# Kernel tuning notes

Measured on AMD Instinct MI355X. Metric: run time of the kernel, lower is better.

## Reference

```python
import jax, jax.numpy as jnp
import numpy as np

N, E = 50000, 400000
C_IN, C_OUT = 64, 32
K = 9  # kernel_size 3x3


def _quad_basis(t):
    # open B-spline basis, degree 2, per torch_spline_conv: k_mod in {0,1,2}
    # t = frac(pseudo * (kernel_size - degree)) = pseudo here (kernel_size=3, degree=2)
    return jnp.stack([0.5 * (1.0 - t) ** 2, -t * t + t + 0.5, 0.5 * t * t], axis=-1)  # [E,3]


def spline_basis(pseudo):
    # kernel_size=[3,3], degree=2, open spline: v = p*(3-2)=p, floor(v)=0 for p in [0,1),
    # so weight index for combination s is exactly s = k_mod0 + 3*k_mod1.
    q0 = _quad_basis(pseudo[:, 0])  # [E,3] varies with s%3
    q1 = _quad_basis(pseudo[:, 1])  # [E,3] varies with s//3
    return (q1[:, :, None] * q0[:, None, :]).reshape(-1, K)  # [E,9]


def spline_conv(x, src, dst, B, W, root, bias, n_nodes):
    xj = x[src]  # gather source node features [E,Cin]
    msg = jnp.zeros((xj.shape[0], W.shape[-1]), x.dtype)
    for k in range(K):  # fixed small kernel loop; avoids [E,K,Cin] blowup
        msg = msg + (xj * B[:, k, None]) @ W[k]
    agg = jax.ops.segment_sum(msg, dst, num_segments=n_nodes)  # aggr='add'
    return agg + x @ root + bias


def setup_inputs() -> dict:
    key = jax.random.key(0)
    ks = jax.random.split(key, 10)
    x = jax.random.normal(ks[0], (N, C_IN), jnp.float32)
    edge_index = jax.random.randint(ks[1], (2, E), 0, N, jnp.int64)
    pseudo = jax.random.uniform(ks[2], (E, 2), jnp.float32)
    skip = jax.random.normal(ks[3], (N, C_OUT), jnp.float32)
    s1 = 1.0 / np.sqrt(C_IN)
    s2 = 1.0 / np.sqrt(C_OUT)
    W1 = jax.random.normal(ks[4], (K, C_IN, C_OUT), jnp.float32) * s1
    root1 = jax.random.normal(ks[5], (C_IN, C_OUT), jnp.float32) * s1
    b1 = jnp.zeros((C_OUT,), jnp.float32)
    W2 = jax.random.normal(ks[6], (K, C_OUT, C_OUT), jnp.float32) * s2
    root2 = jax.random.normal(ks[7], (C_OUT, C_OUT), jnp.float32) * s2
    b2 = jnp.zeros((C_OUT,), jnp.float32)
    return {"x": x, "edge_index": edge_index, "pseudo": pseudo, "skip": skip,
            "W1": W1, "root1": root1, "b1": b1, "W2": W2, "root2": root2, "b2": b2}


def reference(x, edge_index, pseudo, skip, W1, root1, b1, W2, root2, b2):
    src, dst = edge_index[0], edge_index[1]  # flow: source_to_target
    B = spline_basis(pseudo)  # [E,9]
    n = x.shape[0]
    h = jax.nn.relu(spline_conv(x, src, dst, B, W1, root1, b1, n))
    h = jnp.concatenate([h, skip], axis=1)  # [N, Cout+Cskip] == [N, Cin]
    h = jax.nn.relu(spline_conv(h, src, dst, B, W1, root1, b1, n))
    h = jax.nn.relu(spline_conv(h, src, dst, B, W2, root2, b2, n))
    return h
```

## Files before the change

kernel.cpp:

```cpp
#include <hip/hip_runtime.h>
#include <hip/hip_bf16.h>


typedef __attribute__((ext_vector_type(8))) short short8;
typedef __attribute__((ext_vector_type(4))) float f32x4;

__device__ __forceinline__ float blo(unsigned u) {
    union { unsigned u; float f; } x; x.u = u << 16; return x.f;
}
__device__ __forceinline__ float bhi(unsigned u) {
    union { unsigned u; float f; } x; x.u = u & 0xffff0000u; return x.f;
}
__device__ __forceinline__ unsigned short f2bf(float f) {
    union { float f; unsigned u; } x; x.f = f;
    unsigned r = x.u + 0x7fffu + ((x.u >> 16) & 1u);
    return (unsigned short)(r >> 16);
}
__device__ __forceinline__ short8 cvt8(const float* p) {
    float4 a = *(const float4*)p;
    float4 b = *(const float4*)(p + 4);
    short8 r;
    r[0] = (short)f2bf(a.x); r[1] = (short)f2bf(a.y);
    r[2] = (short)f2bf(a.z); r[3] = (short)f2bf(a.w);
    r[4] = (short)f2bf(b.x); r[5] = (short)f2bf(b.y);
    r[6] = (short)f2bf(b.z); r[7] = (short)f2bf(b.w);
    return r;
}

#define YROW 296

__device__ __forceinline__ void m_edge(const unsigned short* sY, const float4 r,
                                       uint4* __restrict__ msgOut, int n0, int l)
{
    const int srcl = __float_as_int(r.x) - n0;
    const int dp   = __float_as_int(r.y);
    const float p0 = r.z, p1 = r.w;

    const float qb[3] = {0.5f * (1.f - p0) * (1.f - p0), -p0 * p0 + p0 + 0.5f, 0.5f * p0 * p0};
    const float qa[3] = {0.5f * (1.f - p1) * (1.f - p1), -p1 * p1 + p1 + 0.5f, 0.5f * p1 * p1};

    const uint4* yb = (const uint4*)(sY + srcl * YROW) + l;
    float s[8] = {0.f, 0.f, 0.f, 0.f, 0.f, 0.f, 0.f, 0.f};
    #pragma unroll
    for (int a = 0; a < 3; ++a) {
        float z[8] = {0.f, 0.f, 0.f, 0.f, 0.f, 0.f, 0.f, 0.f};
        #pragma unroll
        for (int b = 0; b < 3; ++b) {
            uint4 v = yb[(a * 3 + b) * 4];
            const float cw = qb[b];
            z[0] = fmaf(cw, blo(v.x), z[0]); z[1] = fmaf(cw, bhi(v.x), z[1]);
            z[2] = fmaf(cw, blo(v.y), z[2]); z[3] = fmaf(cw, bhi(v.y), z[3]);
            z[4] = fmaf(cw, blo(v.z), z[4]); z[5] = fmaf(cw, bhi(v.z), z[5]);
            z[6] = fmaf(cw, blo(v.w), z[6]); z[7] = fmaf(cw, bhi(v.w), z[7]);
        }
        #pragma unroll
        for (int j = 0; j < 8; ++j) s[j] = fmaf(qa[a], z[j], s[j]);
    }

    union { uint4 u; __hip_bfloat162 h[4]; } o;
    #pragma unroll
    for (int j = 0; j < 4; ++j)
        o.h[j] = __float22bfloat162_rn(float2{s[2 * j], s[2 * j + 1]});
    msgOut[(size_t)dp * 4 + l] = o.u;
}

__device__ __forceinline__ void m_phase(const unsigned short* sY,
                                        const int* __restrict__ sstart,
                                        const float4* __restrict__ erec,
                                        uint4* __restrict__ msgOut,
                                        int n0, int t, int N, int E)
{
    const int e0 = sstart[n0];
    const int e1 = (n0 + 32 < N) ? sstart[n0 + 32] : E;
    const int l  = t & 3;

    int e = e0 + (t >> 2);
    if (e >= e1) return;
    float4 r0 = erec[e];
    bool  has1 = (e + 64 < e1);
    float4 r1;
    if (has1) r1 = erec[e + 64];

    while (true) {
        const int ep0 = e + 128, ep1 = e + 192;
        const bool hp0 = ep0 < e1, hp1 = ep1 < e1;
        float4 rp0, rp1;
        if (hp0) rp0 = erec[ep0];
        if (hp1) rp1 = erec[ep1];

        m_edge(sY, r0, msgOut, n0, l);
        if (!has1) break;
        m_edge(sY, r1, msgOut, n0, l);

        if (!hp0) break;
        r0 = rp0; r1 = rp1; has1 = hp1; e = ep0;
    }
}

template<int NHALF>
__device__ __forceinline__ void t_core(short8 a0, short8 a1,
                                       const unsigned short* __restrict__ Wt,
                                       const float* __restrict__ bias,
                                       unsigned short* sY, float* __restrict__ aggOut,
                                       int n0, int rh, int cgp, int lc, int q, int N)
{
    const int CIN = NHALF * 32;
    #pragma unroll
    for (int j = 0; j < 10; ++j) {
        const int ti = cgp * 10 + j;
        const unsigned short* wp = Wt + ((size_t)(ti * 16 + lc)) * CIN + q * 8;
        f32x4 acc = (f32x4){0.f, 0.f, 0.f, 0.f};
        acc = __builtin_amdgcn_mfma_f32_16x16x32_bf16(a0, *(const short8*)wp, acc, 0, 0, 0);
        if (NHALF == 2)
            acc = __builtin_amdgcn_mfma_f32_16x16x32_bf16(a1, *(const short8*)(wp + 32), acc, 0, 0, 0);

        if (ti < 18) {
            #pragma unroll
            for (int r = 0; r < 4; ++r) {
                int nl = rh * 16 + q * 4 + r;
                sY[nl * YROW + ti * 16 + lc] = f2bf(acc[r]);
            }
        } else {
            int c = (ti - 18) * 16 + lc;
            float bv = bias[c];
            #pragma unroll
            for (int r = 0; r < 4; ++r) {
                int n = n0 + rh * 16 + q * 4 + r;
                if (n < N) aggOut[(size_t)n * 32 + c] = acc[r] + bv;
            }
        }
    }
}

__global__ __launch_bounds__(256, 6)
void layer_tm0(const float* __restrict__ Xa,
               const unsigned short* __restrict__ Wt, const float* __restrict__ bias,
               const int* __restrict__ sstart, const float4* __restrict__ erec,
               float* __restrict__ aggOut, uint4* __restrict__ msgOut, int N, int E)
{
    __shared__ __align__(16) unsigned short sY[32 * YROW];
    const int t = threadIdx.x, wv = t >> 6, lane = t & 63;
    const int lc = lane & 15, q = lane >> 4;
    const int rh = wv & 1, cgp = wv >> 1;
    const int n0 = blockIdx.x * 32;

    int na = n0 + rh * 16 + lc;
    if (na >= N) na = N - 1;
    const float* p = Xa + (size_t)na * 64 + q * 8;
    short8 a0 = cvt8(p);
    short8 a1 = cvt8(p + 32);

    t_core<2>(a0, a1, Wt, bias, sY, aggOut, n0, rh, cgp, lc, q, N);
    __syncthreads();
    m_phase(sY, sstart, erec, msgOut, n0, t, N, E);
}

template<int MODE>
__global__ __launch_bounds__(256, 6)
void layer_gtm(const float* __restrict__ aggPrev, const float* __restrict__ skipv,
               const unsigned short* __restrict__ Wt, const float* __restrict__ bias,
               const int* __restrict__ sstart, const int* __restrict__ dstart,
               const float4* __restrict__ erec,
               const uint4* __restrict__ msgIn, uint4* __restrict__ msgOut,
               float* __restrict__ aggOut, int N, int E)
{
    __shared__ __align__(16) unsigned short sY[32 * YROW];
    float* sH = (float*)sY;
    const int t = threadIdx.x, wv = t >> 6, lane = t & 63;
    const int lc = lane & 15, q = lane >> 4;
    const int rh = wv & 1, cgp = wv >> 1;
    const int n0 = blockIdx.x * 32;

    {
        const int nl = t >> 3;
        const int l  = t & 3;
        const int h  = (t >> 2) & 1;
        int n = n0 + nl;
        if (n >= N) n = N - 1;
        float4 A, B;
        if (h == 0) {
            const float* ap = aggPrev + (size_t)n * 32 + l * 8;
            A = *(const float4*)ap;
            B = *(const float4*)(ap + 4);
        } else {
            A = {0.f, 0.f, 0.f, 0.f};
            B = {0.f, 0.f, 0.f, 0.f};
        }
        float4 C = {0.f, 0.f, 0.f, 0.f}, D = {0.f, 0.f, 0.f, 0.f};
        const int e0 = dstart[n] - E;
        const int e1 = ((n + 1 < N) ? dstart[n + 1] : 2 * E) - E;
        const uint4* mp = msgIn + l;
        int e = e0 + h;
        for (; e + 6 < e1; e += 8) {
            uint4 v0 = mp[(size_t)e * 4];
            uint4 v1 = mp[(size_t)(e + 2) * 4];
            uint4 v2 = mp[(size_t)(e + 4) * 4];
            uint4 v3 = mp[(size_t)(e + 6) * 4];
            A.x += blo(v0.x); A.y += bhi(v0.x); A.z += blo(v0.y); A.w += bhi(v0.y);
            B.x += blo(v0.z); B.y += bhi(v0.z); B.z += blo(v0.w); B.w += bhi(v0.w);
            C.x += blo(v1.x); C.y += bhi(v1.x); C.z += blo(v1.y); C.w += bhi(v1.y);
            D.x += blo(v1.z); D.y += bhi(v1.z); D.z += blo(v1.w); D.w += bhi(v1.w);
            A.x += blo(v2.x); A.y += bhi(v2.x); A.z += blo(v2.y); A.w += bhi(v2.y);
            B.x += blo(v2.z); B.y += bhi(v2.z); B.z += blo(v2.w); B.w += bhi(v2.w);
            C.x += blo(v3.x); C.y += bhi(v3.x); C.z += blo(v3.y); C.w += bhi(v3.y);
            D.x += blo(v3.z); D.y += bhi(v3.z); D.z += blo(v3.w); D.w += bhi(v3.w);
        }
        for (; e < e1; e += 2) {
            uint4 v = mp[(size_t)e * 4];
            A.x += blo(v.x); A.y += bhi(v.x); A.z += blo(v.y); A.w += bhi(v.y);
            B.x += blo(v.z); B.y += bhi(v.z); B.z += blo(v.w); B.w += bhi(v.w);
        }
        A.x += C.x; A.y += C.y; A.z += C.z; A.w += C.w;
        B.x += D.x; B.y += D.y; B.z += D.z; B.w += D.w;
        A.x += __shfl_xor(A.x, 4); A.y += __shfl_xor(A.y, 4);
        A.z += __shfl_xor(A.z, 4); A.w += __shfl_xor(A.w, 4);
        B.x += __shfl_xor(B.x, 4); B.y += __shfl_xor(B.y, 4);
        B.z += __shfl_xor(B.z, 4); B.w += __shfl_xor(B.w, 4);
        if (h == 0) {
            float* hp = sH + nl * 33 + l * 8;
            hp[0] = fmaxf(A.x, 0.f); hp[1] = fmaxf(A.y, 0.f);
            hp[2] = fmaxf(A.z, 0.f); hp[3] = fmaxf(A.w, 0.f);
            hp[4] = fmaxf(B.x, 0.f); hp[5] = fmaxf(B.y, 0.f);
            hp[6] = fmaxf(B.z, 0.f); hp[7] = fmaxf(B.w, 0.f);
        }
    }
    __syncthreads();

    const float* hp = sH + (rh * 16 + lc) * 33 + q * 8;
    union { short8 v; __hip_bfloat162 h2[4]; } pk;
    #pragma unroll
    for (int j = 0; j < 4; ++j)
        pk.h2[j] = __float22bfloat162_rn(float2{hp[2 * j], hp[2 * j + 1]});
    short8 a0 = pk.v;
    short8 a1;
    if (MODE == 1) {
        int na = n0 + rh * 16 + lc;
        if (na >= N) na = N - 1;
        a1 = cvt8(skipv + (size_t)na * 32 + q * 8);
    }
    __syncthreads();

    t_core<(MODE == 1) ? 2 : 1>(a0, a1, Wt, bias, sY, aggOut, n0, rh, cgp, lc, q, N);
    __syncthreads();
    m_phase(sY, sstart, erec, msgOut, n0, t, N, E);
}

__global__ __launch_bounds__(256)
void gather_kernel(const int* __restrict__ dstart, const uint4* __restrict__ msg4,
                   float* __restrict__ agg, int N, int E)
{
    const int t = threadIdx.x;
    const int n = blockIdx.x * 32 + (t >> 3);
    if (n >= N) return;
    const int l = t & 3;
    const int h = (t >> 2) & 1;

    const int e0 = dstart[n] - E;
    const int e1 = ((n + 1 < N) ? dstart[n + 1] : 2 * E) - E;

    float4* ap = (float4*)(agg + (size_t)n * 32 + l * 8);
    float4 A, B;
    if (h == 0) { A = ap[0]; B = ap[1]; }
    else { A = {0.f, 0.f, 0.f, 0.f}; B = {0.f, 0.f, 0.f, 0.f}; }
    float4 C = {0.f, 0.f, 0.f, 0.f}, D = {0.f, 0.f, 0.f, 0.f};
    const uint4* mp = msg4 + l;
    int e = e0 + h;
    for (; e + 6 < e1; e += 8) {
        uint4 v0 = mp[(size_t)e * 4];
        uint4 v1 = mp[(size_t)(e + 2) * 4];
        uint4 v2 = mp[(size_t)(e + 4) * 4];
        uint4 v3 = mp[(size_t)(e + 6) * 4];
        A.x += blo(v0.x); A.y += bhi(v0.x); A.z += blo(v0.y); A.w += bhi(v0.y);
        B.x += blo(v0.z); B.y += bhi(v0.z); B.z += blo(v0.w); B.w += bhi(v0.w);
        C.x += blo(v1.x); C.y += bhi(v1.x); C.z += blo(v1.y); C.w += bhi(v1.y);
        D.x += blo(v1.z); D.y += bhi(v1.z); D.z += blo(v1.w); D.w += bhi(v1.w);
        A.x += blo(v2.x); A.y += bhi(v2.x); A.z += blo(v2.y); A.w += bhi(v2.y);
        B.x += blo(v2.z); B.y += bhi(v2.z); B.z += blo(v2.w); B.w += bhi(v2.w);
        C.x += blo(v3.x); C.y += bhi(v3.x); C.z += blo(v3.y); C.w += bhi(v3.y);
        D.x += blo(v3.z); D.y += bhi(v3.z); D.z += blo(v3.w); D.w += bhi(v3.w);
    }
    for (; e < e1; e += 2) {
        uint4 v = mp[(size_t)e * 4];
        A.x += blo(v.x); A.y += bhi(v.x); A.z += blo(v.y); A.w += bhi(v.y);
        B.x += blo(v.z); B.y += bhi(v.z); B.z += blo(v.w); B.w += bhi(v.w);
    }
    A.x += C.x; A.y += C.y; A.z += C.z; A.w += C.w;
    B.x += D.x; B.y += D.y; B.z += D.z; B.w += D.w;
    A.x += __shfl_xor(A.x, 4); A.y += __shfl_xor(A.y, 4);
    A.z += __shfl_xor(A.z, 4); A.w += __shfl_xor(A.w, 4);
    B.x += __shfl_xor(B.x, 4); B.y += __shfl_xor(B.y, 4);
    B.z += __shfl_xor(B.z, 4); B.w += __shfl_xor(B.w, 4);
    if (h == 0) {
        A.x = fmaxf(A.x, 0.f); A.y = fmaxf(A.y, 0.f); A.z = fmaxf(A.z, 0.f); A.w = fmaxf(A.w, 0.f);
        B.x = fmaxf(B.x, 0.f); B.y = fmaxf(B.y, 0.f); B.z = fmaxf(B.z, 0.f); B.w = fmaxf(B.w, 0.f);
        ap[0] = A; ap[1] = B;
    }
}


__global__ __launch_bounds__(256)
void init_kernel(int* __restrict__ hist, int n2,
                 const float* __restrict__ W1, const float* __restrict__ root1,
                 const float* __restrict__ W2, const float* __restrict__ root2,
                 unsigned short* __restrict__ Wt1, unsigned short* __restrict__ Wt2)
{
    int i = blockIdx.x * 256 + threadIdx.x;
    if (i < n2) { hist[i] = 0; return; }
    int j = i - n2;
    if (j < 320 * 64) {
        int col = j / 64, k = j % 64;
        float v = (col < 288) ? W1[((size_t)(col >> 5) * 64 + k) * 32 + (col & 31)]
                              : root1[(size_t)k * 32 + (col - 288)];
        Wt1[j] = f2bf(v);
    } else if (j < 320 * 96) {
        int jj = j - 320 * 64;
        int col = jj / 32, k = jj % 32;
        float v = (col < 288) ? W2[((size_t)(col >> 5) * 32 + k) * 32 + (col & 31)]
                              : root2[(size_t)k * 32 + (col - 288)];
        Wt2[jj] = f2bf(v);
    }
}

__global__ __launch_bounds__(256)
void count_rank_kernel(const int* __restrict__ ei, int* __restrict__ hist,
                       uint2* __restrict__ rank, int N, int E)
{
    int e = blockIdx.x * 256 + threadIdx.x;
    if (e >= E) return;
    unsigned rs = atomicAdd((unsigned*)&hist[ei[e]], 1u);
    unsigned rd = atomicAdd((unsigned*)&hist[N + ei[E + e]], 1u);
    rank[e] = uint2{rs, rd};
}

__global__ __launch_bounds__(1024)
void scan1_kernel(int* __restrict__ hist, int* __restrict__ bsum, int n)
{
    __shared__ int s[1024];
    int tid = threadIdx.x;
    int i = blockIdx.x * 1024 + tid;
    int v = (i < n) ? hist[i] : 0;
    s[tid] = v;
    __syncthreads();
    for (int off = 1; off < 1024; off <<= 1) {
        int add = (tid >= off) ? s[tid - off] : 0;
        __syncthreads();
        s[tid] += add;
        __syncthreads();
    }
    if (i < n) hist[i] = s[tid] - v;
    if (tid == 1023) bsum[blockIdx.x] = s[1023];
}

__global__ __launch_bounds__(1024)
void scan3_kernel(int* __restrict__ hist, const int* __restrict__ bsum, int n)
{
    __shared__ int sred[128];
    int tid = threadIdx.x;
    int b = blockIdx.x;
    if (tid < 128) sred[tid] = (tid < b) ? bsum[tid] : 0;
    __syncthreads();
    for (int off = 64; off > 0; off >>= 1) {
        if (tid < off) sred[tid] += sred[tid + off];
        __syncthreads();
    }
    int pre = sred[0];
    int i = b * 1024 + tid;
    if (i < n) hist[i] += pre;
}

__global__ __launch_bounds__(256)
void scatter_plain_kernel(const int* __restrict__ ei, const float* __restrict__ pseudo,
                          const int* __restrict__ start, const uint2* __restrict__ rank,
                          float4* __restrict__ erec, int N, int E)
{
    int e = blockIdx.x * 256 + threadIdx.x;
    if (e >= E) return;
    int sv = ei[e];
    int dv = ei[E + e];
    uint2 rk = rank[e];
    int ps = start[sv] + (int)rk.x;
    int pd = start[N + dv] + (int)rk.y - E;
    float4 r;
    r.x = __int_as_float(sv);
    r.y = __int_as_float(pd);
    r.z = pseudo[2 * (size_t)e];
    r.w = pseudo[2 * (size_t)e + 1];
    erec[ps] = r;
}

extern "C" void kernel_launch(void* const* d_in, const int* in_sizes, int n_in,
                              void* d_out, int out_size, void* d_ws, size_t ws_size,
                              hipStream_t stream) {
    const float* x      = (const float*)d_in[0];
    const int*   ei     = (const int*)  d_in[1];
    const float* pseudo = (const float*)d_in[2];
    const float* skip   = (const float*)d_in[3];
    const float* W1     = (const float*)d_in[4];
    const float* root1  = (const float*)d_in[5];
    const float* b1     = (const float*)d_in[6];
    const float* W2     = (const float*)d_in[7];
    const float* root2  = (const float*)d_in[8];
    const float* b2     = (const float*)d_in[9];

    const int N = in_sizes[0] / 64;
    const int E = in_sizes[1] / 2;
    float* out = (float*)d_out;

    unsigned short* msgA = (unsigned short*)d_ws;
    unsigned short* msgB = msgA + (size_t)E * 32;
    float*  agg1  = (float*)(msgB + (size_t)E * 32);
    float*  agg2  = agg1 + (size_t)N * 32;
    float4* erec  = (float4*)(agg2 + (size_t)N * 32);
    int*    start = (int*)(erec + E);
    int*    bsum  = start + 2 * N;
    unsigned short* Wt1 = (unsigned short*)(bsum + 256);
    unsigned short* Wt2 = Wt1 + 320 * 64;
    uint2*  rank  = (uint2*)msgB;

    const dim3 blk(256);
    const int tb   = (N + 31) / 32;
    const int gb   = (N + 31) / 32;
    const int e256 = (E + 255) / 256;
    const int n2k  = (2 * N + 1023) / 1024;
    const int itot = 2 * N + 320 * 96;
    int* dstart = start + N;

    init_kernel<<<(itot + 255) / 256, blk, 0, stream>>>(start, 2 * N, W1, root1, W2, root2, Wt1, Wt2);
    count_rank_kernel<<<e256, blk, 0, stream>>>(ei, start, rank, N, E);
    scan1_kernel<<<n2k, 1024, 0, stream>>>(start, bsum, 2 * N);
    scan3_kernel<<<n2k, 1024, 0, stream>>>(start, bsum, 2 * N);
    scatter_plain_kernel<<<e256, blk, 0, stream>>>(ei, pseudo, start, rank, erec, N, E);

    layer_tm0<<<tb, blk, 0, stream>>>(x, Wt1, b1, start, erec, agg1, (uint4*)msgA, N, E);
    layer_gtm<1><<<tb, blk, 0, stream>>>(agg1, skip, Wt1, b1, start, dstart, erec,
                                         (const uint4*)msgA, (uint4*)msgB, agg2, N, E);
    layer_gtm<2><<<tb, blk, 0, stream>>>(agg2, nullptr, Wt2, b2, start, dstart, erec,
                                         (const uint4*)msgB, (uint4*)msgA, out, N, E);
    gather_kernel<<<gb, blk, 0, stream>>>(dstart, (const uint4*)msgA, out, N, E);
}
```

Baseline: 226.0 us.

## Split fused transform+message kernels into separate transform and message kernels via global Y buffer

Each layer's fused kernel, which computed the per-node transformed features into shared memory and then emitted per-edge messages, is split in two. One kernel writes the bf16 transformed features to a global buffer, and a separate kernel reloads them into shared memory before running the message phase. This lowers per-kernel shared memory and register pressure, and the launch bounds are raised to allow more resident blocks. The cost is extra global traffic for the roughly N×288 bf16 buffer plus three additional kernel launches.

After: 264.8 us. 1.17x slower.

```diff
diff --git a/kernel.cpp b/kernel.cpp
--- a/kernel.cpp
+++ b/kernel.cpp
@@ -28,6 +28,7 @@
 }
 
 #define YROW 296
+#define YGR  288
 
 __device__ __forceinline__ void m_edge(const unsigned short* sY, const float4 r,
                                        uint4* __restrict__ msgOut, int n0, int l)
@@ -98,11 +99,12 @@
 }
 
 template<int NHALF>
-__device__ __forceinline__ void t_core(short8 a0, short8 a1,
-                                       const unsigned short* __restrict__ Wt,
-                                       const float* __restrict__ bias,
-                                       unsigned short* sY, float* __restrict__ aggOut,
-                                       int n0, int rh, int cgp, int lc, int q, int N)
+__device__ __forceinline__ void t_core_g(short8 a0, short8 a1,
+                                         const unsigned short* __restrict__ Wt,
+                                         const float* __restrict__ bias,
+                                         unsigned short* __restrict__ ybuf,
+                                         float* __restrict__ aggOut,
+                                         int n0, int rh, int cgp, int lc, int q, int N)
 {
     const int CIN = NHALF * 32;
     #pragma unroll
@@ -117,8 +119,8 @@
         if (ti < 18) {
             #pragma unroll
             for (int r = 0; r < 4; ++r) {
-                int nl = rh * 16 + q * 4 + r;
-                sY[nl * YROW + ti * 16 + lc] = f2bf(acc[r]);
+                int n = n0 + rh * 16 + q * 4 + r;
+                if (n < N) ybuf[(size_t)n * YGR + ti * 16 + lc] = f2bf(acc[r]);
             }
         } else {
             int c = (ti - 18) * 16 + lc;
@@ -132,13 +134,11 @@
     }
 }
 
-__global__ __launch_bounds__(256, 6)
-void layer_tm0(const float* __restrict__ Xa,
-               const unsigned short* __restrict__ Wt, const float* __restrict__ bias,
-               const int* __restrict__ sstart, const float4* __restrict__ erec,
-               float* __restrict__ aggOut, uint4* __restrict__ msgOut, int N, int E)
-{
-    __shared__ __align__(16) unsigned short sY[32 * YROW];
+__global__ __launch_bounds__(256, 8)
+void layer_t0(const float* __restrict__ Xa,
+              const unsigned short* __restrict__ Wt, const float* __restrict__ bias,
+              unsigned short* __restrict__ ybuf, float* __restrict__ aggOut, int N)
+{
     const int t = threadIdx.x, wv = t >> 6, lane = t & 63;
     const int lc = lane & 15, q = lane >> 4;
     const int rh = wv & 1, cgp = wv >> 1;
@@ -150,22 +150,19 @@
     short8 a0 = cvt8(p);
     short8 a1 = cvt8(p + 32);
 
-    t_core<2>(a0, a1, Wt, bias, sY, aggOut, n0, rh, cgp, lc, q, N);
-    __syncthreads();
-    m_phase(sY, sstart, erec, msgOut, n0, t, N, E);
+    t_core_g<2>(a0, a1, Wt, bias, ybuf, aggOut, n0, rh, cgp, lc, q, N);
 }
 
 template<int MODE>
-__global__ __launch_bounds__(256, 6)
-void layer_gtm(const float* __restrict__ aggPrev, const float* __restrict__ skipv,
-               const unsigned short* __restrict__ Wt, const float* __restrict__ bias,
-               const int* __restrict__ sstart, const int* __restrict__ dstart,
-               const float4* __restrict__ erec,
-               const uint4* __restrict__ msgIn, uint4* __restrict__ msgOut,
-               float* __restrict__ aggOut, int N, int E)
-{
-    __shared__ __align__(16) unsigned short sY[32 * YROW];
-    float* sH = (float*)sY;
+__global__ __launch_bounds__(256, 8)
+void layer_gt(const float* __restrict__ aggPrev, const float* __restrict__ skipv,
+              const unsigned short* __restrict__ Wt, const float* __restrict__ bias,
+              const int* __restrict__ dstart,
+              const uint4* __restrict__ msgIn,
+              unsigned short* __restrict__ ybuf, float* __restrict__ aggOut,
+              int N, int E)
+{
+    __shared__ __align__(16) float sH[32 * 33];
     const int t = threadIdx.x, wv = t >> 6, lane = t & 63;
     const int lc = lane & 15, q = lane >> 4;
     const int rh = wv & 1, cgp = wv >> 1;
@@ -238,10 +235,31 @@
         if (na >= N) na = N - 1;
         a1 = cvt8(skipv + (size_t)na * 32 + q * 8);
     }
+
+    t_core_g<(MODE == 1) ? 2 : 1>(a0, a1, Wt, bias, ybuf, aggOut, n0, rh, cgp, lc, q, N);
+}
+
+__global__ __launch_bounds__(256, 8)
+void layer_m(const unsigned short* __restrict__ ybuf,
+             const int* __restrict__ sstart, const float4* __restrict__ erec,
+             uint4* __restrict__ msgOut, int N, int E)
+{
+    __shared__ __align__(16) unsigned short sY[32 * YROW];
+    const int t = threadIdx.x;
+    const int n0 = blockIdx.x * 32;
+
+    #pragma unroll
+    for (int k = 0; k < 9; ++k) {
+        int idx = t + k * 256;
+        int row = idx / 72;
+        int c2  = idx - row * 72;
+        int n = n0 + row;
+        if (n >= N) n = N - 1;
+        *(uint2*)(sY + row * YROW + c2 * 4) =
+            *(const uint2*)(ybuf + (size_t)n * YGR + c2 * 4);
+    }
     __syncthreads();
 
-    t_core<(MODE == 1) ? 2 : 1>(a0, a1, Wt, bias, sY, aggOut, n0, rh, cgp, lc, q, N);
-    __syncthreads();
     m_phase(sY, sstart, erec, msgOut, n0, t, N, E);
 }
 
@@ -408,7 +426,8 @@
 
     unsigned short* msgA = (unsigned short*)d_ws;
     unsigned short* msgB = msgA + (size_t)E * 32;
-    float*  agg1  = (float*)(msgB + (size_t)E * 32);
+    unsigned short* ybuf = msgB + (size_t)E * 32;
+    float*  agg1  = (float*)(ybuf + (size_t)N * YGR);
     float*  agg2  = agg1 + (size_t)N * 32;
     float4* erec  = (float4*)(agg2 + (size_t)N * 32);
     int*    start = (int*)(erec + E);
@@ -431,10 +450,13 @@
     scan3_kernel<<<n2k, 1024, 0, stream>>>(start, bsum, 2 * N);
     scatter_plain_kernel<<<e256, blk, 0, stream>>>(ei, pseudo, start, rank, erec, N, E);
 
-    layer_tm0<<<tb, blk, 0, stream>>>(x, Wt1, b1, start, erec, agg1, (uint4*)msgA, N, E);
-    layer_gtm<1><<<tb, blk, 0, stream>>>(agg1, skip, Wt1, b1, start, dstart, erec,
-                                         (const uint4*)msgA, (uint4*)msgB, agg2, N, E);
-    layer_gtm<2><<<tb, blk, 0, stream>>>(agg2, nullptr, Wt2, b2, start, dstart, erec,
-                                         (const uint4*)msgB, (uint4*)msgA, out, N, E);
+    layer_t0<<<tb, blk, 0, stream>>>(x, Wt1, b1, ybuf, agg1, N);
+    layer_m<<<tb, blk, 0, stream>>>(ybuf, start, erec, (uint4*)msgA, N, E);
+    layer_gt<1><<<tb, blk, 0, stream>>>(agg1, skip, Wt1, b1, dstart,
+                                        (const uint4*)msgA, ybuf, agg2, N, E);
+    layer_m<<<tb, blk, 0, stream>>>(ybuf, start, erec, (uint4*)msgB, N, E);
+    layer_gt<2><<<tb, blk, 0, stream>>>(agg2, nullptr, Wt2, b2, dstart,
+                                        (const uint4*)msgB, ybuf, out, N, E);
+    layer_m<<<tb, blk, 0, stream>>>(ybuf, start, erec, (uint4*)msgA, N, E);
     gather_kernel<<<gb, blk, 0, stream>>>(dstart, (const uint4*)msgA, out, N, E);
 }
```
